# Performance work log

Hardware: AMD Instinct MI355X
Metric: run time of the kernel (lower is better)

The kernel has to match this reference:

```python
import jax, jax.numpy as jnp
from jax import lax
import numpy as np

# Dcls2_1d config (matches init_kwargs)
K_H, K_W = 3, 3          # base kernel size
DIL = 4                  # max dilation along dim 0 (learnable spacings)
LIM = DIL // 2           # each tap may move +/- LIM rows
KH_EFF = K_H + 2 * LIM   # constructed kernel height (7)
PAD_H = 1 + LIM          # user padding 1 adjusted by dilation//2 (as in _adjust_padding)
PAD_W = 1


def build_kernel(weight, P1):
    """Construct dense conv kernel by bilinear scatter of weights at
    continuous learnable row offsets P1. weight,P1: (O, I, K_H, K_W).
    Returns (O, I, KH_EFF, K_W)."""
    kh = jnp.arange(K_H, dtype=weight.dtype)[None, None, :, None]
    pos = kh + LIM + jnp.clip(P1, -LIM, LIM)      # continuous row position in [0, KH_EFF-1]
    p0 = jnp.floor(pos)
    frac = pos - p0                                # interpolation residual (grad flows to P)
    p0i = p0.astype(jnp.int32)
    oh0 = jax.nn.one_hot(p0i, KH_EFF, dtype=weight.dtype)        # (O,I,Kh,Kw,KH_EFF)
    oh1 = jax.nn.one_hot(p0i + 1, KH_EFF, dtype=weight.dtype)    # OOB rows -> all-zero row
    return (jnp.einsum('oihw,oihwk->oikw', weight * (1.0 - frac), oh0)
            + jnp.einsum('oihw,oihwk->oikw', weight * frac, oh1))


def setup_inputs() -> dict:
    key = jax.random.key(0)
    k1, k2, k3, k4 = jax.random.split(key, 4)
    x = jax.random.normal(k1, (16, 128, 64, 64), jnp.float32)
    weight = jax.random.normal(k2, (256, 128, 3, 3), jnp.float32) * 0.03
    bias = jax.random.normal(k3, (256,), jnp.float32) * 0.01
    # learnable positions span the allowed +/- LIM range to exercise interpolation
    P = jax.random.uniform(k4, (1, 256, 128, 3, 3), jnp.float32, -2.0, 2.0)
    return {"x": x, "weight": weight, "bias": bias, "P": P}


def reference(x, weight, bias, P):
    K = build_kernel(weight, P[0])
    out = lax.conv_general_dilated(
        x, K,
        window_strides=(1, 1),
        padding=((PAD_H, PAD_H), (PAD_W, PAD_W)),
        dimension_numbers=('NCHW', 'OIHW', 'NCHW'),
        feature_group_count=1)
    return out + bias[None, :, None, None]
```

## Files before the change

kernel.cpp:

```cpp
#include <hip/hip_runtime.h>
#include <hip/hip_bf16.h>

#define NIMG 16
#define CIN 128
#define COUT 256
#define HH 64
#define WW 64
#define KHE 7
#define KW_ 3
#define HP (HH + 6)
#define WP (WW + 2)
#define KDIM (CIN * KHE * KW_)
#define NKT 42

typedef __attribute__((ext_vector_type(8))) short short8;
typedef __attribute__((ext_vector_type(4))) float f32x4;

#define AS1(p) ((const __attribute__((address_space(1))) void*)(p))
#define AS3(p) ((__attribute__((address_space(3))) void*)(p))

__global__ void __launch_bounds__(256) pad_convert(const float* __restrict__ x,
                                                   ushort* __restrict__ xp) {
  const int bid = blockIdx.x;
  const int n = bid / HP, hp = bid % HP;
  const int h = hp - 3;
  ushort* dst = xp + (size_t)(n * HP + hp) * (WP * CIN);
  const int tid = threadIdx.x;

  if (h < 0 || h >= HH) {
    uint4* p = (uint4*)dst;
    uint4 z; z.x = z.y = z.z = z.w = 0u;
    for (int idx = tid; idx < (WP * CIN * 2) / 16; idx += 256) p[idx] = z;
    return;
  }

  __shared__ ushort t[CIN][WW + 1];
  for (int it = 0; it < (CIN * WW) / 256; ++it) {
    int flat = it * 256 + tid;
    int i = flat >> 6, w = flat & 63;
    float v = x[(((size_t)n * CIN + i) * HH + h) * WW + w];
    __hip_bfloat16 b = __float2bfloat16(v);
    t[i][w] = *(ushort*)&b;
  }
  __syncthreads();
  for (int it = 0; it < (WP * CIN) / 256; ++it) {
    int flat = it * 256 + tid;
    int wp = flat >> 7, i = flat & 127;
    int w = wp - 1;
    ushort v = (w < 0 || w >= WW) ? (ushort)0 : t[i][w];
    dst[flat] = v;
  }
}

__global__ void __launch_bounds__(256) build_kb(const float* __restrict__ weight,
                                                const float* __restrict__ P,
                                                ushort* __restrict__ kb2) {
  int idx = blockIdx.x * 256 + threadIdx.x;
  if (idx >= COUT * KW_ * CIN) return;
  int i = idx & 127;
  int kw = (idx >> 7) % 3;
  int o = idx / (KW_ * CIN);
  int base = (o * CIN + i) * 9 + kw;

  float a[KHE] = {0.f, 0.f, 0.f, 0.f, 0.f, 0.f, 0.f};
#pragma unroll
  for (int kh = 0; kh < 3; ++kh) {
    float wv = weight[base + kh * 3];
    float p = P[base + kh * 3];
    p = fminf(2.f, fmaxf(-2.f, p));
    float pos = (float)(kh + 2) + p;
    float fl = floorf(pos);
    float fr = pos - fl;
    int r0 = (int)fl;
    float c0 = wv * (1.f - fr);
    float c1 = wv * fr;
#pragma unroll
    for (int r = 0; r < KHE; ++r) {
      a[r] += ((r0 == r) ? c0 : 0.f) + ((r0 + 1 == r) ? c1 : 0.f);
    }
  }
#pragma unroll
  for (int r = 0; r < KHE; ++r) {
    __hip_bfloat16 b = __float2bfloat16(a[r]);
    int kslice = (r * 3 + kw) * 4 + (i >> 5);
    kb2[(size_t)kslice * 8192 + o * 32 + (i & 31)] = *(ushort*)&b;
  }
}

__global__ void __launch_bounds__(512, 2) dcls_gemm(const ushort* __restrict__ xp,
                                                    const ushort* __restrict__ kb2,
                                                    const float* __restrict__ bias,
                                                    float* __restrict__ out) {
  __shared__ __align__(16) ushort As[4][256 * 64];

  const int tid = threadIdx.x;
  const int lane = tid & 63;
  const int wv = tid >> 6;
  const int wr = wv >> 2;
  const int wc = wv & 3;
  const int g = lane >> 4;
  const int lm = lane & 15;
  const int m0 = blockIdx.x << 8;

  const int srow = tid >> 3;
  const int swz = ((tid & 7) ^ (srow & 7)) * 8;

  const ushort* pA[4];
#pragma unroll
  for (int j = 0; j < 4; ++j) {
    int r = j * 64 + srow;
    int m = m0 + r;
    int ni = m >> 12, hh = (m >> 6) & 63, ww = m & 63;
    pA[j] = xp + (size_t)((ni * HP + hh) * WP + ww) * CIN + swz;
  }

  const ushort* kbB = kb2 + (size_t)wc * 2048 + lm * 32 + g * 8;

#define STAGEA(buf, kt) do { \
    int kh_ = (kt) / 6; int rem_ = (kt) - kh_ * 6; \
    int kw2_ = rem_ >> 1; int ic_ = rem_ & 1; \
    int offA_ = (kh_ * WP + kw2_) * CIN + ic_ * 64; \
    _Pragma("unroll") \
    for (int j_ = 0; j_ < 4; ++j_) \
      __builtin_amdgcn_global_load_lds(AS1(pA[j_] + offA_), AS3(&As[buf][(j_ * 64 + wv * 8) * 64]), 16, 0, 0); \
  } while (0)

#define LOADB(dst, kt) do { \
    _Pragma("unroll") \
    for (int n_ = 0; n_ < 4; ++n_) \
      _Pragma("unroll") \
      for (int kk_ = 0; kk_ < 2; ++kk_) \
        dst[n_][kk_] = *(const short8*)(kbB + (size_t)((kt) * 2 + kk_) * 8192 + n_ * 512); \
  } while (0)

  f32x4 acc[8][4] = {};
  const int swzR = (lm & 7) << 4;

  short8 bf0[4][2], bf1[4][2];
  short8 afp[4], afq[4];

#define READ_AF(dst, Ab, half, kk) do { \
    _Pragma("unroll") \
    for (int m4_ = 0; m4_ < 4; ++m4_) { \
      int rowA_ = wr * 128 + (half) * 64 + m4_ * 16 + lm; \
      dst[m4_] = *(const short8*)((Ab) + rowA_ * 128 + (((kk) * 64 + g * 16) ^ swzR)); \
    } \
  } while (0)

#define MFMA_G(afv, bfc, half, kk) do { \
    __builtin_amdgcn_s_setprio(1); \
    _Pragma("unroll") \
    for (int m4_ = 0; m4_ < 4; ++m4_) \
      _Pragma("unroll") \
      for (int n_ = 0; n_ < 4; ++n_) \
        acc[(half) * 4 + m4_][n_] = __builtin_amdgcn_mfma_f32_16x16x32_bf16( \
            afv[m4_], bfc[n_][kk], acc[(half) * 4 + m4_][n_], 0, 0, 0); \
    __builtin_amdgcn_s_setprio(0); \
  } while (0)

#define LGKM_GATE(n) do { \
    __builtin_amdgcn_sched_barrier(0); \
    asm volatile("s_waitcnt lgkmcnt(" #n ")" ::: "memory"); \
    __builtin_amdgcn_sched_barrier(0); \
  } while (0)

#define SUBITER(kt, bfc) do { \
    __builtin_amdgcn_sched_barrier(0); \
    asm volatile("s_waitcnt vmcnt(12)" ::: "memory"); \
    __builtin_amdgcn_s_barrier(); \
    __builtin_amdgcn_sched_barrier(0); \
    int ktn_ = ((kt) + 2 < NKT) ? (kt) + 2 : 0; \
    STAGEA(((kt) + 2) & 3, ktn_); \
    const char* Ab = (const char*)&As[(kt) & 3][0]; \
    READ_AF(afp, Ab, 0, 0); \
    READ_AF(afq, Ab, 0, 1); \
    LGKM_GATE(4); \
    MFMA_G(afp, bfc, 0, 0); \
    READ_AF(afp, Ab, 1, 0); \
    LGKM_GATE(4); \
    MFMA_G(afq, bfc, 0, 1); \
    READ_AF(afq, Ab, 1, 1); \
    LGKM_GATE(4); \
    MFMA_G(afp, bfc, 1, 0); \
    LGKM_GATE(0); \
    MFMA_G(afq, bfc, 1, 1); \
    LOADB(bfc, ktn_); \
  } while (0)

  STAGEA(0, 0);
  LOADB(bf0, 0);
  STAGEA(1, 1);
  LOADB(bf1, 1);

  for (int kt = 0; kt < NKT; kt += 2) {
    SUBITER(kt, bf0);
    SUBITER(kt + 1, bf1);
  }
#undef SUBITER
#undef LGKM_GATE
#undef MFMA_G
#undef READ_AF
#undef LOADB
#undef STAGEA

#pragma unroll
  for (int n_ = 0; n_ < 4; ++n_)
#pragma unroll
    for (int kk_ = 0; kk_ < 2; ++kk_) {
      asm volatile("" :: "v"((int)bf0[n_][kk_][0]));
      asm volatile("" :: "v"((int)bf1[n_][kk_][0]));
    }

#pragma unroll
  for (int fn = 0; fn < 4; ++fn) {
    int o = wc * 64 + fn * 16 + lm;
    float bv = bias[o];
#pragma unroll
    for (int fm = 0; fm < 8; ++fm) {
      int m = m0 + wr * 128 + fm * 16 + g * 4;
      int ni = m >> 12, hh = (m >> 6) & 63, ww = m & 63;
      f32x4 v = acc[fm][fn];
      v[0] += bv; v[1] += bv; v[2] += bv; v[3] += bv;
      *(f32x4*)(out + (size_t)((ni * COUT + o) * HH + hh) * WW + ww) = v;
    }
  }
}

extern "C" void kernel_launch(void* const* d_in, const int* in_sizes, int n_in,
                              void* d_out, int out_size, void* d_ws, size_t ws_size,
                              hipStream_t stream) {
  const float* x = (const float*)d_in[0];
  const float* weight = (const float*)d_in[1];
  const float* bias = (const float*)d_in[2];
  const float* P = (const float*)d_in[3];
  float* out = (float*)d_out;

  const size_t xp_elems = (size_t)NIMG * HP * WP * CIN;
  ushort* xp = (ushort*)d_ws;
  ushort* kb2 = (ushort*)((char*)d_ws + xp_elems * 2);

  hipLaunchKernelGGL(pad_convert, dim3(NIMG * HP), dim3(256), 0, stream, x, xp);
  hipLaunchKernelGGL(build_kb, dim3((COUT * KW_ * CIN + 255) / 256), dim3(256), 0, stream,
                     weight, P, kb2);
  hipLaunchKernelGGL(dcls_gemm, dim3(65536 / 256), dim3(512), 0, stream, xp, kb2, bias, out);
}
```

Measured before the change: 96.07 us.

## Interleave A-tile staging and B loads with MFMA groups using per-phase barriers

```diff
diff --git a/kernel.cpp b/kernel.cpp
--- a/kernel.cpp
+++ b/kernel.cpp
@@ -116,51 +116,56 @@
 
   const ushort* kbB = kb2 + (size_t)wc * 2048 + lm * 32 + g * 8;
 
-#define STAGEA(buf, kt) do { \
+#define STAGEA1(buf, kt, j_) do { \
     int kh_ = (kt) / 6; int rem_ = (kt) - kh_ * 6; \
     int kw2_ = rem_ >> 1; int ic_ = rem_ & 1; \
     int offA_ = (kh_ * WP + kw2_) * CIN + ic_ * 64; \
-    _Pragma("unroll") \
-    for (int j_ = 0; j_ < 4; ++j_) \
-      __builtin_amdgcn_global_load_lds(AS1(pA[j_] + offA_), AS3(&As[buf][(j_ * 64 + wv * 8) * 64]), 16, 0, 0); \
-  } while (0)
-
-#define LOADB(dst, kt) do { \
+    __builtin_amdgcn_global_load_lds(AS1(pA[j_] + offA_), AS3(&As[buf][((j_) * 64 + wv * 8) * 64]), 16, 0, 0); \
+  } while (0)
+
+#define LOADB_K(dst, kt, kk_) do { \
     _Pragma("unroll") \
     for (int n_ = 0; n_ < 4; ++n_) \
-      _Pragma("unroll") \
-      for (int kk_ = 0; kk_ < 2; ++kk_) \
-        dst[n_][kk_] = *(const short8*)(kbB + (size_t)((kt) * 2 + kk_) * 8192 + n_ * 512); \
-  } while (0)
+      dst[n_][kk_] = *(const short8*)(kbB + (size_t)((kt) * 2 + (kk_)) * 8192 + n_ * 512); \
+  } while (0)
+
+#define LOADB(dst, kt) do { LOADB_K(dst, kt, 0); LOADB_K(dst, kt, 1); } while (0)
 
   f32x4 acc[8][4] = {};
   const int swzR = (lm & 7) << 4;
 
   short8 bf0[4][2], bf1[4][2];
-  short8 afp[4], afq[4];
-
-#define READ_AF(dst, Ab, half, kk) do { \
+  short8 af[4];
+
+#define READ_AF(Ab, half, kk) do { \
     _Pragma("unroll") \
     for (int m4_ = 0; m4_ < 4; ++m4_) { \
       int rowA_ = wr * 128 + (half) * 64 + m4_ * 16 + lm; \
-      dst[m4_] = *(const short8*)((Ab) + rowA_ * 128 + (((kk) * 64 + g * 16) ^ swzR)); \
+      af[m4_] = *(const short8*)((Ab) + rowA_ * 128 + (((kk) * 64 + g * 16) ^ swzR)); \
     } \
   } while (0)
 
-#define MFMA_G(afv, bfc, half, kk) do { \
+#define MFMA_G(bfc, half, kk) do { \
     __builtin_amdgcn_s_setprio(1); \
     _Pragma("unroll") \
     for (int m4_ = 0; m4_ < 4; ++m4_) \
       _Pragma("unroll") \
       for (int n_ = 0; n_ < 4; ++n_) \
         acc[(half) * 4 + m4_][n_] = __builtin_amdgcn_mfma_f32_16x16x32_bf16( \
-            afv[m4_], bfc[n_][kk], acc[(half) * 4 + m4_][n_], 0, 0, 0); \
+            af[m4_], bfc[n_][kk], acc[(half) * 4 + m4_][n_], 0, 0, 0); \
     __builtin_amdgcn_s_setprio(0); \
   } while (0)
 
-#define LGKM_GATE(n) do { \
-    __builtin_amdgcn_sched_barrier(0); \
-    asm volatile("s_waitcnt lgkmcnt(" #n ")" ::: "memory"); \
+#define BARLG do { \
+    __builtin_amdgcn_sched_barrier(0); \
+    __builtin_amdgcn_s_barrier(); \
+    asm volatile("s_waitcnt lgkmcnt(0)" ::: "memory"); \
+    __builtin_amdgcn_sched_barrier(0); \
+  } while (0)
+
+#define BAR do { \
+    __builtin_amdgcn_sched_barrier(0); \
+    __builtin_amdgcn_s_barrier(); \
     __builtin_amdgcn_sched_barrier(0); \
   } while (0)
 
@@ -170,26 +175,21 @@
     __builtin_amdgcn_s_barrier(); \
     __builtin_amdgcn_sched_barrier(0); \
     int ktn_ = ((kt) + 2 < NKT) ? (kt) + 2 : 0; \
-    STAGEA(((kt) + 2) & 3, ktn_); \
+    int buf_ = ((kt) + 2) & 3; \
     const char* Ab = (const char*)&As[(kt) & 3][0]; \
-    READ_AF(afp, Ab, 0, 0); \
-    READ_AF(afq, Ab, 0, 1); \
-    LGKM_GATE(4); \
-    MFMA_G(afp, bfc, 0, 0); \
-    READ_AF(afp, Ab, 1, 0); \
-    LGKM_GATE(4); \
-    MFMA_G(afq, bfc, 0, 1); \
-    READ_AF(afq, Ab, 1, 1); \
-    LGKM_GATE(4); \
-    MFMA_G(afp, bfc, 1, 0); \
-    LGKM_GATE(0); \
-    MFMA_G(afq, bfc, 1, 1); \
-    LOADB(bfc, ktn_); \
-  } while (0)
-
-  STAGEA(0, 0);
+     READ_AF(Ab, 0, 0); STAGEA1(buf_, ktn_, 0); \
+    BARLG; MFMA_G(bfc, 0, 0); BAR; \
+     READ_AF(Ab, 0, 1); STAGEA1(buf_, ktn_, 1); \
+    BARLG; MFMA_G(bfc, 0, 1); BAR; \
+     READ_AF(Ab, 1, 0); STAGEA1(buf_, ktn_, 2); \
+    BARLG; MFMA_G(bfc, 1, 0); LOADB_K(bfc, ktn_, 0); BAR; \
+     READ_AF(Ab, 1, 1); STAGEA1(buf_, ktn_, 3); \
+    BARLG; MFMA_G(bfc, 1, 1); LOADB_K(bfc, ktn_, 1); \
+  } while (0)
+
+  STAGEA1(0, 0, 0); STAGEA1(0, 0, 1); STAGEA1(0, 0, 2); STAGEA1(0, 0, 3);
   LOADB(bf0, 0);
-  STAGEA(1, 1);
+  STAGEA1(1, 1, 0); STAGEA1(1, 1, 1); STAGEA1(1, 1, 2); STAGEA1(1, 1, 3);
   LOADB(bf1, 1);
 
   for (int kt = 0; kt < NKT; kt += 2) {
@@ -197,11 +197,13 @@
     SUBITER(kt + 1, bf1);
   }
 #undef SUBITER
-#undef LGKM_GATE
+#undef BAR
+#undef BARLG
 #undef MFMA_G
 #undef READ_AF
 #undef LOADB
-#undef STAGEA
+#undef LOADB_K
+#undef STAGEA1
 
 #pragma unroll
   for (int n_ = 0; n_ < 4; ++n_)
```

Result: slower. 99.63 us (+3.7%).
